# Optimization experiments

Measured on AMD Instinct MI355X. Metric: run time of the kernel, lower is better.

The kernel has to match this reference:

```python
import jax, jax.numpy as jnp
import numpy as np

N = 2048
FEAT = 64 + 512 + 4096 + 32768 + 192 + 216  # 37848 actual concat width

# 54 neighbor offsets: dx,dy,dz in {-1,0,1}, dt in {-1,1}
_OFFSETS = np.array([[dx, dy, dz, dt]
                     for dx in (-1, 0, 1)
                     for dy in (-1, 0, 1)
                     for dz in (-1, 0, 1)
                     for dt in (-1, 1)], dtype=np.int32)


def setup_inputs() -> dict:
    key = jax.random.key(0)
    ks = jax.random.split(key, 12)
    pos = jax.random.uniform(ks[0], (N, 3), dtype=jnp.float32)
    dir = jax.random.normal(ks[1], (N, 3), dtype=jnp.float32)
    t = jax.random.uniform(ks[2], (N,), dtype=jnp.float32)
    table0 = jax.random.normal(ks[3], (128, 128, 128, 64), dtype=jnp.float32)
    table1 = jax.random.normal(ks[4], (64, 64, 64, 512), dtype=jnp.float32)
    table2 = jax.random.normal(ks[5], (32, 32, 32, 4096), dtype=jnp.float32)
    table3 = jax.random.normal(ks[6], (16, 16, 16, 32768), dtype=jnp.float32)
    ts_table1 = jax.random.normal(ks[7], (16, 16, 16, 64, 64), dtype=jnp.float32)
    ts_table2 = jax.random.normal(ks[8], (128, 128, 128, 128, 4), dtype=jnp.float32)
    W_mlp = jax.random.normal(ks[9], (128, FEAT), dtype=jnp.float32) * 0.01
    W_proj = jax.random.normal(ks[10], (4, 132), dtype=jnp.float32) * 0.1
    b_proj = jnp.zeros((4,), dtype=jnp.float32)
    return dict(pos=pos, dir=dir, t=t, table0=table0, table1=table1,
                table2=table2, table3=table3, ts_table1=ts_table1,
                ts_table2=ts_table2, W_mlp=W_mlp, W_proj=W_proj, b_proj=b_proj)


def _gather3(table, idx):
    return table[idx[:, 0], idx[:, 1], idx[:, 2]]


def reference(pos, dir, t, table0, table1, table2, table3,
              ts_table1, ts_table2, W_mlp, W_proj, b_proj):
    idx0 = (pos * 127).astype(jnp.int32)
    idx1 = (pos * 63).astype(jnp.int32)
    idx2 = (pos * 31).astype(jnp.int32)
    idx3 = (pos * 15).astype(jnp.int32)
    t_idx = (t * 127).astype(jnp.int32)            # [N]
    idx4 = jnp.concatenate([idx3, t_idx[:, None]], axis=-1)  # [N,4]

    f0 = _gather3(table0, idx0)   # [N,64]
    f1 = _gather3(table1, idx1)   # [N,512]
    f2 = _gather3(table2, idx2)   # [N,4096]
    f3 = _gather3(table3, idx3)   # [N,32768]

    # time table: spatial idx3, time index wrapped mod 64 for delta in {-1,0,1}
    def ts1(delta):
        ti = jnp.mod(t_idx + delta, 64)
        return ts_table1[idx3[:, 0], idx3[:, 1], idx3[:, 2], ti]  # [N,64]
    time_feats = jnp.concatenate([ts1(-1), ts1(0), ts1(1)], axis=-1)  # [N,192]

    # 54 modulo-wrapped 4D neighbor lookups, vectorized
    dims4 = jnp.array([128, 128, 128, 128], dtype=jnp.int32)
    nb = jnp.mod(idx4[:, None, :] + jnp.asarray(_OFFSETS)[None, :, :], dims4)  # [N,54,4]
    nb_feats = ts_table2[nb[..., 0], nb[..., 1], nb[..., 2], nb[..., 3]]       # [N,54,4]
    nb_feats = nb_feats.reshape(nb_feats.shape[0], -1)                          # [N,216]

    all_feats = jnp.concatenate([f0, f1, f2, f3, time_feats, nb_feats], axis=-1)  # [N,37848]
    all_feats = jax.nn.relu(all_feats)  # F.relu then model_sequence ReLU (idempotent)
    downsized = all_feats @ W_mlp.T     # [N,128]

    final = jnp.concatenate([downsized, dir, t[:, None]], axis=-1)  # [N,132]
    return final @ W_proj.T + b_proj     # [N,4]
```

## Files before the change

kernel.cpp:

```cpp
#include <hip/hip_runtime.h>


#define N_PTS 2048
#define KP_TOTAL 37888
#define K_ORIG 37848
#define KSPLIT_M 20
#define KS3 4
#define FOLD_BLOCKS 592

__global__ __launch_bounds__(1024) void mark_kernel(const float* __restrict__ pos,
                                                    int* __restrict__ list,
                                                    int* __restrict__ count) {
    __shared__ int flags[4096];
    __shared__ int cnt;
    const int tid = threadIdx.x;
    for (int i = tid; i < 4096; i += 1024) flags[i] = 0;
    if (tid == 0) cnt = 0;
    __syncthreads();
    #pragma unroll
    for (int q = 0; q < 2; ++q) {
        const int n = q * 1024 + tid;
        const float px = pos[3 * n], py = pos[3 * n + 1], pz = pos[3 * n + 2];
        const int i3 = (int)(px * 15.f), j3 = (int)(py * 15.f), k3 = (int)(pz * 15.f);
        const int cell = (i3 * 16 + j3) * 16 + k3;
        if (atomicExch(&flags[cell], 1) == 0) {
            const int p = atomicAdd(&cnt, 1);
            list[p] = cell;
        }
    }
    __syncthreads();
    if (tid == 0) count[0] = cnt;
}

__global__ __launch_bounds__(256) void setup_kernel(
    const float* __restrict__ Wm, const float* __restrict__ Wproj,
    float* __restrict__ Wf,
    const float* __restrict__ pos, const float* __restrict__ t,
    const float* __restrict__ table0, const float* __restrict__ table1,
    const float* __restrict__ ts1, const float* __restrict__ ts2,
    float* __restrict__ dense, int* __restrict__ bases) {

    const int b = blockIdx.x;
    const int tid = threadIdx.x;

    if (b < FOLD_BLOCKS) {
        __shared__ float red[4][64][4];
        const int kpl = tid & 63;
        const int jq  = tid >> 6;
        const int kp  = b * 64 + kpl;
        int k; bool valid = true;
        if (kp < 576)        k = kp;
        else if (kp < 768)   k = 37440 + (kp - 576);
        else if (kp < 984)   k = 37632 + (kp - 768);
        else if (kp < 1024)  { k = 0; valid = false; }
        else if (kp < 5120)  k = 576 + (kp - 1024);
        else                 k = 4672 + (kp - 5120);
        float a0 = 0.f, a1 = 0.f, a2 = 0.f, a3 = 0.f;
        if (valid) {
            const float* wk = Wm + k;
            const int j0 = jq * 32;
            #pragma unroll
            for (int jj = 0; jj < 32; ++jj) {
                const int j = j0 + jj;
                const float w = wk[(size_t)j * K_ORIG];
                a0 = fmaf(Wproj[0 * 132 + j], w, a0);
                a1 = fmaf(Wproj[1 * 132 + j], w, a1);
                a2 = fmaf(Wproj[2 * 132 + j], w, a2);
                a3 = fmaf(Wproj[3 * 132 + j], w, a3);
            }
        }
        red[jq][kpl][0] = a0; red[jq][kpl][1] = a1;
        red[jq][kpl][2] = a2; red[jq][kpl][3] = a3;
        __syncthreads();
        const int rkpl = tid >> 2, rch = tid & 3;
        const float s = red[0][rkpl][rch] + red[1][rkpl][rch]
                      + red[2][rkpl][rch] + red[3][rkpl][rch];
        Wf[(size_t)rch * KP_TOTAL + b * 64 + rkpl] = s;
        return;
    }

    const int n = b - FOLD_BLOCKS;
    const float px = pos[3 * n], py = pos[3 * n + 1], pz = pos[3 * n + 2];
    const float tv = t[n];
    const int i0 = (int)(px * 127.f), j0 = (int)(py * 127.f), k0 = (int)(pz * 127.f);
    const int i1 = (int)(px * 63.f),  j1 = (int)(py * 63.f),  k1 = (int)(pz * 63.f);
    const int i2 = (int)(px * 31.f),  j2 = (int)(py * 31.f),  k2 = (int)(pz * 31.f);
    const int i3 = (int)(px * 15.f),  j3 = (int)(py * 15.f),  k3 = (int)(pz * 15.f);
    const int ti = (int)(tv * 127.f);

    float* drow = dense + (size_t)n * 1024;

    if (tid < 64)
        drow[tid] = table0[(size_t)(((i0 * 128 + j0) * 128 + k0)) * 64 + tid];
    #pragma unroll
    for (int e = tid; e < 512; e += 256)
        drow[64 + e] = table1[(size_t)(((i1 * 64 + j1) * 64 + k1)) * 512 + e];
    if (tid < 192) {
        const int d = tid >> 6, e = tid & 63;
        const int tw = (ti + d - 1 + 64) & 63;
        drow[576 + tid] = ts1[((size_t)(((i3 * 16 + j3) * 16 + k3)) * 64 + tw) * 64 + e];
    }
    if (tid < 216) {
        const int o = tid >> 2, cc = tid & 3;
        const int dt_ = (o & 1) ? 1 : -1;
        const int rest = o >> 1;
        const int dz_ = rest % 3 - 1;
        const int dy_ = (rest / 3) % 3 - 1;
        const int dx_ = rest / 9 - 1;
        const int x = (i3 + dx_ + 128) & 127;
        const int y = (j3 + dy_ + 128) & 127;
        const int z = (k3 + dz_ + 128) & 127;
        const int w = (ti + dt_ + 128) & 127;
        drow[768 + tid] = ts2[(((((size_t)x * 128 + y) * 128 + z) * 128 + w) * 4) + cc];
    } else if (tid >= 216 && tid < 256) {
        drow[768 + tid] = 0.f;
    }
    if (tid == 0) {
        bases[2 * n]     = ((i2 * 32 + j2) * 32 + k2) * 4096;
        bases[2 * n + 1] = ((i3 * 16 + j3) * 16 + k3) * 32768;
    }
}

__global__ __launch_bounds__(256) void celldot_kernel(
    const float* __restrict__ table3, const float* __restrict__ Wf,
    const int* __restrict__ list, const int* __restrict__ count,
    float* __restrict__ cellpart) {

    const int cnt = count[0];
    const int yb = blockIdx.y;
    if (yb * 4 >= cnt) return;
    const int ks = blockIdx.x;
    const int tid = threadIdx.x;

    int cell[4]; const float* rowp[4]; bool val[4];
    #pragma unroll
    for (int j = 0; j < 4; ++j) {
        const int idx = yb * 4 + j;
        val[j] = idx < cnt;
        cell[j] = list[val[j] ? idx : 0];
        rowp[j] = table3 + (size_t)cell[j] * 32768;
    }

    const int qbase = ks * 8192;
    const float* wf0 = Wf + (size_t)0 * KP_TOTAL + 5120 + qbase;
    const float* wf1 = Wf + (size_t)1 * KP_TOTAL + 5120 + qbase;
    const float* wf2 = Wf + (size_t)2 * KP_TOTAL + 5120 + qbase;
    const float* wf3 = Wf + (size_t)3 * KP_TOTAL + 5120 + qbase;

    float accv[4][4];
    #pragma unroll
    for (int j = 0; j < 4; ++j)
        #pragma unroll
        for (int c = 0; c < 4; ++c) accv[j][c] = 0.f;

    #pragma unroll 2
    for (int kk = 0; kk < 8; ++kk) {
        const int off = kk * 1024 + tid * 4;
        const float4 w0 = *(const float4*)(wf0 + off);
        const float4 w1 = *(const float4*)(wf1 + off);
        const float4 w2 = *(const float4*)(wf2 + off);
        const float4 w3 = *(const float4*)(wf3 + off);
        #pragma unroll
        for (int j = 0; j < 4; ++j) {
            float4 r = *(const float4*)(rowp[j] + qbase + off);
            r.x = fmaxf(r.x, 0.f); r.y = fmaxf(r.y, 0.f);
            r.z = fmaxf(r.z, 0.f); r.w = fmaxf(r.w, 0.f);
            accv[j][0] = fmaf(r.x, w0.x, fmaf(r.y, w0.y, fmaf(r.z, w0.z, fmaf(r.w, w0.w, accv[j][0]))));
            accv[j][1] = fmaf(r.x, w1.x, fmaf(r.y, w1.y, fmaf(r.z, w1.z, fmaf(r.w, w1.w, accv[j][1]))));
            accv[j][2] = fmaf(r.x, w2.x, fmaf(r.y, w2.y, fmaf(r.z, w2.z, fmaf(r.w, w2.w, accv[j][2]))));
            accv[j][3] = fmaf(r.x, w3.x, fmaf(r.y, w3.y, fmaf(r.z, w3.z, fmaf(r.w, w3.w, accv[j][3]))));
        }
    }

    #pragma unroll
    for (int s = 1; s < 64; s <<= 1)
        #pragma unroll
        for (int j = 0; j < 4; ++j)
            #pragma unroll
            for (int c = 0; c < 4; ++c)
                accv[j][c] += __shfl_xor(accv[j][c], s);

    __shared__ float red[4][16];
    const int wv = tid >> 6, ln = tid & 63;
    if (ln == 0)
        #pragma unroll
        for (int j = 0; j < 4; ++j)
            #pragma unroll
            for (int c = 0; c < 4; ++c)
                red[wv][j * 4 + c] = accv[j][c];
    __syncthreads();
    if (tid < 16) {
        const float s = red[0][tid] + red[1][tid] + red[2][tid] + red[3][tid];
        const int j = tid >> 2, c = tid & 3;
        if (val[j])
            cellpart[((size_t)ks * 4096 + cell[j]) * 4 + c] = s;
    }
}

__global__ __launch_bounds__(256) void main_kernel(
    const float* __restrict__ dense, const float* __restrict__ table2,
    const int* __restrict__ bases,
    const float* __restrict__ Wf, float* __restrict__ part) {

    const int ks = blockIdx.x;
    const int mb = blockIdx.y;
    const int tid = threadIdx.x;
    const int p = tid >> 2;
    const int q = tid & 3;
    const int n = mb * 64 + p;

    const float* drow = dense + (size_t)n * 1024;
    const int f2b = bases[2 * n];
    const int kbase = ks * 256 + q * 8;

    float acc0 = 0.f, acc1 = 0.f, acc2 = 0.f, acc3 = 0.f;

    #pragma unroll 2
    for (int i = 0; i < 8; ++i) {
        const int kp = kbase + i * 32;
        const float* src = (kp < 1024) ? (drow + kp)
                                       : (table2 + (size_t)f2b + (kp - 1024));
        float4 fa = ((const float4*)src)[0];
        float4 fb = ((const float4*)src)[1];
        fa.x = fmaxf(fa.x, 0.f); fa.y = fmaxf(fa.y, 0.f);
        fa.z = fmaxf(fa.z, 0.f); fa.w = fmaxf(fa.w, 0.f);
        fb.x = fmaxf(fb.x, 0.f); fb.y = fmaxf(fb.y, 0.f);
        fb.z = fmaxf(fb.z, 0.f); fb.w = fmaxf(fb.w, 0.f);

        const float4* w0 = (const float4*)(Wf + (size_t)0 * KP_TOTAL + kp);
        const float4* w1 = (const float4*)(Wf + (size_t)1 * KP_TOTAL + kp);
        const float4* w2 = (const float4*)(Wf + (size_t)2 * KP_TOTAL + kp);
        const float4* w3 = (const float4*)(Wf + (size_t)3 * KP_TOTAL + kp);
        float4 wa, wb;
        wa = w0[0]; wb = w0[1];
        acc0 = fmaf(wa.x, fa.x, fmaf(wa.y, fa.y, fmaf(wa.z, fa.z, fmaf(wa.w, fa.w,
               fmaf(wb.x, fb.x, fmaf(wb.y, fb.y, fmaf(wb.z, fb.z, fmaf(wb.w, fb.w, acc0))))))));
        wa = w1[0]; wb = w1[1];
        acc1 = fmaf(wa.x, fa.x, fmaf(wa.y, fa.y, fmaf(wa.z, fa.z, fmaf(wa.w, fa.w,
               fmaf(wb.x, fb.x, fmaf(wb.y, fb.y, fmaf(wb.z, fb.z, fmaf(wb.w, fb.w, acc1))))))));
        wa = w2[0]; wb = w2[1];
        acc2 = fmaf(wa.x, fa.x, fmaf(wa.y, fa.y, fmaf(wa.z, fa.z, fmaf(wa.w, fa.w,
               fmaf(wb.x, fb.x, fmaf(wb.y, fb.y, fmaf(wb.z, fb.z, fmaf(wb.w, fb.w, acc2))))))));
        wa = w3[0]; wb = w3[1];
        acc3 = fmaf(wa.x, fa.x, fmaf(wa.y, fa.y, fmaf(wa.z, fa.z, fmaf(wa.w, fa.w,
               fmaf(wb.x, fb.x, fmaf(wb.y, fb.y, fmaf(wb.z, fb.z, fmaf(wb.w, fb.w, acc3))))))));
    }

    acc0 += __shfl_xor(acc0, 1); acc0 += __shfl_xor(acc0, 2);
    acc1 += __shfl_xor(acc1, 1); acc1 += __shfl_xor(acc1, 2);
    acc2 += __shfl_xor(acc2, 1); acc2 += __shfl_xor(acc2, 2);
    acc3 += __shfl_xor(acc3, 1); acc3 += __shfl_xor(acc3, 2);

    if (q == 0) {
        float4 r; r.x = acc0; r.y = acc1; r.z = acc2; r.w = acc3;
        ((float4*)part)[(size_t)ks * N_PTS + n] = r;
    }
}

__global__ __launch_bounds__(256) void reduce_kernel(
    const float* __restrict__ part, const float* __restrict__ cellpart,
    const int* __restrict__ bases,
    const float* __restrict__ dir, const float* __restrict__ t,
    const float* __restrict__ Wproj, const float* __restrict__ bproj,
    float* __restrict__ out) {
    const int tid = threadIdx.x;
    const int n = blockIdx.x * 64 + (tid >> 2);
    const int c = tid & 3;
    const int cell = bases[2 * n + 1] >> 15;
    float s = 0.f;
    #pragma unroll
    for (int ks = 0; ks < KSPLIT_M; ++ks)
        s += part[((size_t)ks * N_PTS + n) * 4 + c];
    #pragma unroll
    for (int ks = 0; ks < KS3; ++ks)
        s += cellpart[((size_t)ks * 4096 + cell) * 4 + c];
    s += dir[3 * n]     * Wproj[c * 132 + 128];
    s += dir[3 * n + 1] * Wproj[c * 132 + 129];
    s += dir[3 * n + 2] * Wproj[c * 132 + 130];
    s += t[n]           * Wproj[c * 132 + 131];
    s += bproj[c];
    out[n * 4 + c] = s;
}

extern "C" void kernel_launch(void* const* d_in, const int* in_sizes, int n_in,
                              void* d_out, int out_size, void* d_ws, size_t ws_size,
                              hipStream_t stream) {
    const float* pos    = (const float*)d_in[0];
    const float* dir    = (const float*)d_in[1];
    const float* t      = (const float*)d_in[2];
    const float* table0 = (const float*)d_in[3];
    const float* table1 = (const float*)d_in[4];
    const float* table2 = (const float*)d_in[5];
    const float* table3 = (const float*)d_in[6];
    const float* ts1    = (const float*)d_in[7];
    const float* ts2    = (const float*)d_in[8];
    const float* Wm     = (const float*)d_in[9];
    const float* Wproj  = (const float*)d_in[10];
    const float* bproj  = (const float*)d_in[11];
    float* out = (float*)d_out;

    char* ws = (char*)d_ws;
    float* Wf       = (float*)(ws);
    float* dense    = (float*)(ws + 606208);
    int*   bases    = (int*)(ws + 8994816);
    float* part     = (float*)(ws + 9011200);
    float* cellpart = (float*)(ws + 9666560);
    int*   list     = (int*)(ws + 9928704);
    int*   count    = (int*)(ws + 9945088);

    hipLaunchKernelGGL(mark_kernel, dim3(1), dim3(1024), 0, stream, pos, list, count);
    hipLaunchKernelGGL(setup_kernel, dim3(FOLD_BLOCKS + N_PTS), dim3(256), 0, stream,
                       Wm, Wproj, Wf, pos, t, table0, table1, ts1, ts2, dense, bases);
    hipLaunchKernelGGL(celldot_kernel, dim3(KS3, 1024), dim3(256), 0, stream,
                       table3, Wf, list, count, cellpart);
    hipLaunchKernelGGL(main_kernel, dim3(KSPLIT_M, 32), dim3(256), 0, stream,
                       dense, table2, bases, Wf, part);
    hipLaunchKernelGGL(reduce_kernel, dim3(32), dim3(256), 0, stream,
                       part, cellpart, bases, dir, t, Wproj, bproj, out);
}
```

Baseline: 72.85 us.

## Fuse per-point gathers, dot product and final projection into one kernel

```diff
diff --git a/kernel.cpp b/kernel.cpp
--- a/kernel.cpp
+++ b/kernel.cpp
@@ -4,41 +4,13 @@
 #define N_PTS 2048
 #define KP_TOTAL 37888
 #define K_ORIG 37848
-#define KSPLIT_M 20
 #define KS3 4
 #define FOLD_BLOCKS 592
 
-__global__ __launch_bounds__(1024) void mark_kernel(const float* __restrict__ pos,
-                                                    int* __restrict__ list,
-                                                    int* __restrict__ count) {
-    __shared__ int flags[4096];
-    __shared__ int cnt;
-    const int tid = threadIdx.x;
-    for (int i = tid; i < 4096; i += 1024) flags[i] = 0;
-    if (tid == 0) cnt = 0;
-    __syncthreads();
-    #pragma unroll
-    for (int q = 0; q < 2; ++q) {
-        const int n = q * 1024 + tid;
-        const float px = pos[3 * n], py = pos[3 * n + 1], pz = pos[3 * n + 2];
-        const int i3 = (int)(px * 15.f), j3 = (int)(py * 15.f), k3 = (int)(pz * 15.f);
-        const int cell = (i3 * 16 + j3) * 16 + k3;
-        if (atomicExch(&flags[cell], 1) == 0) {
-            const int p = atomicAdd(&cnt, 1);
-            list[p] = cell;
-        }
-    }
-    __syncthreads();
-    if (tid == 0) count[0] = cnt;
-}
-
 __global__ __launch_bounds__(256) void setup_kernel(
     const float* __restrict__ Wm, const float* __restrict__ Wproj,
-    float* __restrict__ Wf,
-    const float* __restrict__ pos, const float* __restrict__ t,
-    const float* __restrict__ table0, const float* __restrict__ table1,
-    const float* __restrict__ ts1, const float* __restrict__ ts2,
-    float* __restrict__ dense, int* __restrict__ bases) {
+    float* __restrict__ Wf, const float* __restrict__ pos,
+    int* __restrict__ list, int* __restrict__ count) {
 
     const int b = blockIdx.x;
     const int tid = threadIdx.x;
@@ -79,46 +51,24 @@
         return;
     }
 
-    const int n = b - FOLD_BLOCKS;
-    const float px = pos[3 * n], py = pos[3 * n + 1], pz = pos[3 * n + 2];
-    const float tv = t[n];
-    const int i0 = (int)(px * 127.f), j0 = (int)(py * 127.f), k0 = (int)(pz * 127.f);
-    const int i1 = (int)(px * 63.f),  j1 = (int)(py * 63.f),  k1 = (int)(pz * 63.f);
-    const int i2 = (int)(px * 31.f),  j2 = (int)(py * 31.f),  k2 = (int)(pz * 31.f);
-    const int i3 = (int)(px * 15.f),  j3 = (int)(py * 15.f),  k3 = (int)(pz * 15.f);
-    const int ti = (int)(tv * 127.f);
-
-    float* drow = dense + (size_t)n * 1024;
-
-    if (tid < 64)
-        drow[tid] = table0[(size_t)(((i0 * 128 + j0) * 128 + k0)) * 64 + tid];
-    #pragma unroll
-    for (int e = tid; e < 512; e += 256)
-        drow[64 + e] = table1[(size_t)(((i1 * 64 + j1) * 64 + k1)) * 512 + e];
-    if (tid < 192) {
-        const int d = tid >> 6, e = tid & 63;
-        const int tw = (ti + d - 1 + 64) & 63;
-        drow[576 + tid] = ts1[((size_t)(((i3 * 16 + j3) * 16 + k3)) * 64 + tw) * 64 + e];
-    }
-    if (tid < 216) {
-        const int o = tid >> 2, cc = tid & 3;
-        const int dt_ = (o & 1) ? 1 : -1;
-        const int rest = o >> 1;
-        const int dz_ = rest % 3 - 1;
-        const int dy_ = (rest / 3) % 3 - 1;
-        const int dx_ = rest / 9 - 1;
-        const int x = (i3 + dx_ + 128) & 127;
-        const int y = (j3 + dy_ + 128) & 127;
-        const int z = (k3 + dz_ + 128) & 127;
-        const int w = (ti + dt_ + 128) & 127;
-        drow[768 + tid] = ts2[(((((size_t)x * 128 + y) * 128 + z) * 128 + w) * 4) + cc];
-    } else if (tid >= 216 && tid < 256) {
-        drow[768 + tid] = 0.f;
-    }
-    if (tid == 0) {
-        bases[2 * n]     = ((i2 * 32 + j2) * 32 + k2) * 4096;
-        bases[2 * n + 1] = ((i3 * 16 + j3) * 16 + k3) * 32768;
-    }
+    __shared__ int flags[4096];
+    __shared__ int cnt;
+    for (int i = tid; i < 4096; i += 256) flags[i] = 0;
+    if (tid == 0) cnt = 0;
+    __syncthreads();
+    #pragma unroll
+    for (int q = 0; q < 8; ++q) {
+        const int n = q * 256 + tid;
+        const float px = pos[3 * n], py = pos[3 * n + 1], pz = pos[3 * n + 2];
+        const int i3 = (int)(px * 15.f), j3 = (int)(py * 15.f), k3 = (int)(pz * 15.f);
+        const int cell = (i3 * 16 + j3) * 16 + k3;
+        if (atomicExch(&flags[cell], 1) == 0) {
+            const int p = atomicAdd(&cnt, 1);
+            list[p] = cell;
+        }
+    }
+    __syncthreads();
+    if (tid == 0) count[0] = cnt;
 }
 
 __global__ __launch_bounds__(256) void celldot_kernel(
@@ -197,89 +147,105 @@
     }
 }
 
-__global__ __launch_bounds__(256) void main_kernel(
-    const float* __restrict__ dense, const float* __restrict__ table2,
-    const int* __restrict__ bases,
-    const float* __restrict__ Wf, float* __restrict__ part) {
-
-    const int ks = blockIdx.x;
-    const int mb = blockIdx.y;
-    const int tid = threadIdx.x;
-    const int p = tid >> 2;
-    const int q = tid & 3;
-    const int n = mb * 64 + p;
-
-    const float* drow = dense + (size_t)n * 1024;
-    const int f2b = bases[2 * n];
-    const int kbase = ks * 256 + q * 8;
-
-    float acc0 = 0.f, acc1 = 0.f, acc2 = 0.f, acc3 = 0.f;
-
-    #pragma unroll 2
-    for (int i = 0; i < 8; ++i) {
-        const int kp = kbase + i * 32;
-        const float* src = (kp < 1024) ? (drow + kp)
-                                       : (table2 + (size_t)f2b + (kp - 1024));
-        float4 fa = ((const float4*)src)[0];
-        float4 fb = ((const float4*)src)[1];
-        fa.x = fmaxf(fa.x, 0.f); fa.y = fmaxf(fa.y, 0.f);
-        fa.z = fmaxf(fa.z, 0.f); fa.w = fmaxf(fa.w, 0.f);
-        fb.x = fmaxf(fb.x, 0.f); fb.y = fmaxf(fb.y, 0.f);
-        fb.z = fmaxf(fb.z, 0.f); fb.w = fmaxf(fb.w, 0.f);
-
-        const float4* w0 = (const float4*)(Wf + (size_t)0 * KP_TOTAL + kp);
-        const float4* w1 = (const float4*)(Wf + (size_t)1 * KP_TOTAL + kp);
-        const float4* w2 = (const float4*)(Wf + (size_t)2 * KP_TOTAL + kp);
-        const float4* w3 = (const float4*)(Wf + (size_t)3 * KP_TOTAL + kp);
-        float4 wa, wb;
-        wa = w0[0]; wb = w0[1];
-        acc0 = fmaf(wa.x, fa.x, fmaf(wa.y, fa.y, fmaf(wa.z, fa.z, fmaf(wa.w, fa.w,
-               fmaf(wb.x, fb.x, fmaf(wb.y, fb.y, fmaf(wb.z, fb.z, fmaf(wb.w, fb.w, acc0))))))));
-        wa = w1[0]; wb = w1[1];
-        acc1 = fmaf(wa.x, fa.x, fmaf(wa.y, fa.y, fmaf(wa.z, fa.z, fmaf(wa.w, fa.w,
-               fmaf(wb.x, fb.x, fmaf(wb.y, fb.y, fmaf(wb.z, fb.z, fmaf(wb.w, fb.w, acc1))))))));
-        wa = w2[0]; wb = w2[1];
-        acc2 = fmaf(wa.x, fa.x, fmaf(wa.y, fa.y, fmaf(wa.z, fa.z, fmaf(wa.w, fa.w,
-               fmaf(wb.x, fb.x, fmaf(wb.y, fb.y, fmaf(wb.z, fb.z, fmaf(wb.w, fb.w, acc2))))))));
-        wa = w3[0]; wb = w3[1];
-        acc3 = fmaf(wa.x, fa.x, fmaf(wa.y, fa.y, fmaf(wa.z, fa.z, fmaf(wa.w, fa.w,
-               fmaf(wb.x, fb.x, fmaf(wb.y, fb.y, fmaf(wb.z, fb.z, fmaf(wb.w, fb.w, acc3))))))));
-    }
-
-    acc0 += __shfl_xor(acc0, 1); acc0 += __shfl_xor(acc0, 2);
-    acc1 += __shfl_xor(acc1, 1); acc1 += __shfl_xor(acc1, 2);
-    acc2 += __shfl_xor(acc2, 1); acc2 += __shfl_xor(acc2, 2);
-    acc3 += __shfl_xor(acc3, 1); acc3 += __shfl_xor(acc3, 2);
-
-    if (q == 0) {
-        float4 r; r.x = acc0; r.y = acc1; r.z = acc2; r.w = acc3;
-        ((float4*)part)[(size_t)ks * N_PTS + n] = r;
-    }
-}
-
-__global__ __launch_bounds__(256) void reduce_kernel(
-    const float* __restrict__ part, const float* __restrict__ cellpart,
-    const int* __restrict__ bases,
-    const float* __restrict__ dir, const float* __restrict__ t,
+__global__ __launch_bounds__(256) void point_kernel(
+    const float* __restrict__ pos, const float* __restrict__ dir,
+    const float* __restrict__ t,
+    const float* __restrict__ table0, const float* __restrict__ table1,
+    const float* __restrict__ table2,
+    const float* __restrict__ ts1, const float* __restrict__ ts2,
+    const float* __restrict__ Wf, const float* __restrict__ cellpart,
     const float* __restrict__ Wproj, const float* __restrict__ bproj,
     float* __restrict__ out) {
+
+    const int n = blockIdx.x;
     const int tid = threadIdx.x;
-    const int n = blockIdx.x * 64 + (tid >> 2);
-    const int c = tid & 3;
-    const int cell = bases[2 * n + 1] >> 15;
-    float s = 0.f;
-    #pragma unroll
-    for (int ks = 0; ks < KSPLIT_M; ++ks)
-        s += part[((size_t)ks * N_PTS + n) * 4 + c];
-    #pragma unroll
-    for (int ks = 0; ks < KS3; ++ks)
-        s += cellpart[((size_t)ks * 4096 + cell) * 4 + c];
-    s += dir[3 * n]     * Wproj[c * 132 + 128];
-    s += dir[3 * n + 1] * Wproj[c * 132 + 129];
-    s += dir[3 * n + 2] * Wproj[c * 132 + 130];
-    s += t[n]           * Wproj[c * 132 + 131];
-    s += bproj[c];
-    out[n * 4 + c] = s;
+
+    const float px = pos[3 * n], py = pos[3 * n + 1], pz = pos[3 * n + 2];
+    const float tv = t[n];
+    const int i0 = (int)(px * 127.f), j0 = (int)(py * 127.f), k0 = (int)(pz * 127.f);
+    const int i1 = (int)(px * 63.f),  j1 = (int)(py * 63.f),  k1 = (int)(pz * 63.f);
+    const int i2 = (int)(px * 31.f),  j2 = (int)(py * 31.f),  k2 = (int)(pz * 31.f);
+    const int i3 = (int)(px * 15.f),  j3 = (int)(py * 15.f),  k3 = (int)(pz * 15.f);
+    const int ti = (int)(tv * 127.f);
+    const int cell = (i3 * 16 + j3) * 16 + k3;
+
+    const float* f0p = table0 + (size_t)((i0 * 128 + j0) * 128 + k0) * 64;
+    const float* f1p = table1 + (size_t)((i1 * 64 + j1) * 64 + k1) * 512;
+    const float* f2p = table2 + (size_t)((i2 * 32 + j2) * 32 + k2) * 4096;
+    const float* t1p = ts1 + (size_t)cell * 4096;
+
+    float a0 = 0.f, a1 = 0.f, a2 = 0.f, a3 = 0.f;
+
+    #pragma unroll
+    for (int s5 = 0; s5 < 5; ++s5) {
+        const int slot = s5 * 256 + tid;
+        float4 f;
+        bool have = true;
+        if (slot >= 256) {
+            f = *(const float4*)(f2p + (slot - 256) * 4);
+        } else if (slot < 16) {
+            f = *(const float4*)(f0p + slot * 4);
+        } else if (slot < 144) {
+            f = *(const float4*)(f1p + (slot - 16) * 4);
+        } else if (slot < 192) {
+            const int s2 = slot - 144;
+            const int d = s2 >> 4;
+            const int e4 = (s2 & 15) * 4;
+            const int tw = (ti + d - 1 + 64) & 63;
+            f = *(const float4*)(t1p + tw * 64 + e4);
+        } else if (slot < 246) {
+            const int o = slot - 192;
+            const int dt_ = (o & 1) ? 1 : -1;
+            const int rest = o >> 1;
+            const int dz_ = rest % 3 - 1;
+            const int dy_ = (rest / 3) % 3 - 1;
+            const int dx_ = rest / 9 - 1;
+            const int x = (i3 + dx_ + 128) & 127;
+            const int y = (j3 + dy_ + 128) & 127;
+            const int z = (k3 + dz_ + 128) & 127;
+            const int w = (ti + dt_ + 128) & 127;
+            f = *(const float4*)(ts2 + ((size_t)((x * 128 + y) * 128 + z) * 128 + w) * 4);
+        } else {
+            have = false;
+        }
+        if (have) {
+            f.x = fmaxf(f.x, 0.f); f.y = fmaxf(f.y, 0.f);
+            f.z = fmaxf(f.z, 0.f); f.w = fmaxf(f.w, 0.f);
+            const int kp = slot * 4;
+            const float4 w0 = *(const float4*)(Wf + (size_t)0 * KP_TOTAL + kp);
+            const float4 w1 = *(const float4*)(Wf + (size_t)1 * KP_TOTAL + kp);
+            const float4 w2 = *(const float4*)(Wf + (size_t)2 * KP_TOTAL + kp);
+            const float4 w3 = *(const float4*)(Wf + (size_t)3 * KP_TOTAL + kp);
+            a0 = fmaf(f.x, w0.x, fmaf(f.y, w0.y, fmaf(f.z, w0.z, fmaf(f.w, w0.w, a0))));
+            a1 = fmaf(f.x, w1.x, fmaf(f.y, w1.y, fmaf(f.z, w1.z, fmaf(f.w, w1.w, a1))));
+            a2 = fmaf(f.x, w2.x, fmaf(f.y, w2.y, fmaf(f.z, w2.z, fmaf(f.w, w2.w, a2))));
+            a3 = fmaf(f.x, w3.x, fmaf(f.y, w3.y, fmaf(f.z, w3.z, fmaf(f.w, w3.w, a3))));
+        }
+    }
+
+    #pragma unroll
+    for (int s = 1; s < 64; s <<= 1) {
+        a0 += __shfl_xor(a0, s);
+        a1 += __shfl_xor(a1, s);
+        a2 += __shfl_xor(a2, s);
+        a3 += __shfl_xor(a3, s);
+    }
+    __shared__ float red[4][4];
+    const int wv = tid >> 6, ln = tid & 63;
+    if (ln == 0) { red[wv][0] = a0; red[wv][1] = a1; red[wv][2] = a2; red[wv][3] = a3; }
+    __syncthreads();
+    if (tid < 4) {
+        float s = red[0][tid] + red[1][tid] + red[2][tid] + red[3][tid];
+        #pragma unroll
+        for (int ks = 0; ks < KS3; ++ks)
+            s += cellpart[((size_t)ks * 4096 + cell) * 4 + tid];
+        s += dir[3 * n]     * Wproj[tid * 132 + 128];
+        s += dir[3 * n + 1] * Wproj[tid * 132 + 129];
+        s += dir[3 * n + 2] * Wproj[tid * 132 + 130];
+        s += tv             * Wproj[tid * 132 + 131];
+        s += bproj[tid];
+        out[n * 4 + tid] = s;
+    }
 }
 
 extern "C" void kernel_launch(void* const* d_in, const int* in_sizes, int n_in,
@@ -301,20 +267,15 @@
 
     char* ws = (char*)d_ws;
     float* Wf       = (float*)(ws);
-    float* dense    = (float*)(ws + 606208);
-    int*   bases    = (int*)(ws + 8994816);
-    float* part     = (float*)(ws + 9011200);
-    float* cellpart = (float*)(ws + 9666560);
-    int*   list     = (int*)(ws + 9928704);
-    int*   count    = (int*)(ws + 9945088);
-
-    hipLaunchKernelGGL(mark_kernel, dim3(1), dim3(1024), 0, stream, pos, list, count);
-    hipLaunchKernelGGL(setup_kernel, dim3(FOLD_BLOCKS + N_PTS), dim3(256), 0, stream,
-                       Wm, Wproj, Wf, pos, t, table0, table1, ts1, ts2, dense, bases);
-    hipLaunchKernelGGL(celldot_kernel, dim3(KS3, 1024), dim3(256), 0, stream,
+    float* cellpart = (float*)(ws + 606208);
+    int*   list     = (int*)(ws + 868352);
+    int*   count    = (int*)(ws + 884736);
+
+    hipLaunchKernelGGL(setup_kernel, dim3(FOLD_BLOCKS + 1), dim3(256), 0, stream,
+                       Wm, Wproj, Wf, pos, list, count);
+    hipLaunchKernelGGL(celldot_kernel, dim3(KS3, 512), dim3(256), 0, stream,
                        table3, Wf, list, count, cellpart);
-    hipLaunchKernelGGL(main_kernel, dim3(KSPLIT_M, 32), dim3(256), 0, stream,
-                       dense, table2, bases, Wf, part);
-    hipLaunchKernelGGL(reduce_kernel, dim3(32), dim3(256), 0, stream,
-                       part, cellpart, bases, dir, t, Wproj, bproj, out);
-}
+    hipLaunchKernelGGL(point_kernel, dim3(N_PTS), dim3(256), 0, stream,
+                       pos, dir, t, table0, table1, table2, ts1, ts2,
+                       Wf, cellpart, Wproj, bproj, out);
+}
```

After: 63.19 us. -13.3%, faster.
